# Optimization experiments

Hardware: AMD Instinct MI355X
Metric: run time of the kernel (lower is better)

## Reference

```python
import jax, jax.numpy as jnp
import numpy as np

B, C, H, W = 4, 3, 96, 96
HW = H * W
IGNORE = 0          # HD_IGNORE_CLASS_INDEX
BIG = 1e9           # stand-in for +inf in masked min


def setup_inputs() -> dict:
    key = jax.random.key(0)
    k1, k2 = jax.random.split(key)
    predictions = jax.random.normal(k1, (B, C, H, W), dtype=jnp.float32)
    labels_int = jax.random.randint(k2, (B, H, W), 0, C, dtype=jnp.int32)
    return {"predictions": predictions, "labels_int": labels_int}


def get_boundary(img):
    # img: [B, C, H, W] binary mask. Faithful to the numpy version (square images):
    # new = img + 4-neighbor sums (zero outside), boundary = img * (5 - new).
    pad = lambda x, spec: jnp.pad(x, ((0, 0), (0, 0)) + spec)
    new = (img
           + pad(img[:, :, 1:, :], ((0, 1), (0, 0)))
           + pad(img[:, :, :-1, :], ((1, 0), (0, 0)))
           + pad(img[:, :, :, 1:], ((0, 0), (0, 1)))
           + pad(img[:, :, :, :-1], ((0, 0), (1, 0))))
    return img * (5.0 - new)


def _pixel_dist_matrix():
    yy, xx = jnp.meshgrid(jnp.arange(H), jnp.arange(W), indexing="ij")
    coords = jnp.stack([yy.ravel(), xx.ravel()], axis=-1).astype(jnp.float32)  # [HW,2] (row,col) like argwhere
    sq = jnp.sum(coords * coords, axis=-1)
    D2 = sq[:, None] + sq[None, :] - 2.0 * (coords @ coords.T)
    return jnp.sqrt(jnp.maximum(D2, 0.0))  # [HW, HW]


def reference(predictions, labels_int):
    labels = jax.nn.one_hot(labels_int, C, axis=1, dtype=jnp.float32)        # [B,C,H,W]
    preds = jax.nn.one_hot(jnp.argmax(predictions, axis=1), C, axis=1,
                           dtype=jnp.float32)                                # [B,C,H,W]

    bd_a = (get_boundary(preds) > 0).astype(jnp.float32)
    bd_b = (get_boundary(labels) > 0).astype(jnp.float32)

    a = preds.reshape(B * C, HW)
    b = labels.reshape(B * C, HW)
    ba = bd_a.reshape(B * C, HW)
    bb = bd_b.reshape(B * C, HW)

    D = _pixel_dist_matrix()  # [HW, HW], shared across all (batch, class) pairs

    def pair(args):
        a_, b_, ba_, bb_ = args
        n_a = a_.sum()
        n_b = b_.sum()
        a_fwd = a_ * (1.0 - b_)   # pred-only pixels (false positive region)
        b_bwd = b_ * (1.0 - a_)   # label-only pixels
        # min distance from every pixel to boundary set, via masked min (no argwhere)
        mins_f = jnp.min(jnp.where(bb_[None, :] > 0, D, BIG), axis=1)  # to boundary(b)
        mins_b = jnp.min(jnp.where(ba_[None, :] > 0, D, BIG), axis=1)  # to boundary(a)
        # mean(min) * |A_fwd| / |a| == sum(min over A_fwd) / |a|
        hd_f = jnp.where((a_fwd.sum() > 0) & (bb_.sum() > 0),
                         jnp.sum(a_fwd * mins_f) / jnp.maximum(n_a, 1.0), 0.0)
        hd_b = jnp.where((b_bwd.sum() > 0) & (ba_.sum() > 0),
                         jnp.sum(b_bwd * mins_b) / jnp.maximum(n_b, 1.0), 0.0)
        hd = jnp.maximum(hd_f, hd_b)
        # empty prediction mask -> failure case (ignore_failed_hd = False => (h+w)/4)
        hd = jnp.where(n_a > 0, hd, (H + W) / 4.0)
        return hd, (n_a == 0).astype(jnp.float32)

    hd_pairs, failed_pairs = jax.lax.map(pair, (a, b, ba, bb))

    hd = hd_pairs.reshape(B, C).at[:, IGNORE].set(0.0)
    failed = failed_pairs.reshape(B, C).sum(axis=0).at[IGNORE].set(0.0)

    HD = jnp.zeros((B, C + 2), dtype=jnp.float32)
    HD = HD.at[:, :C].set(hd)
    HD = HD.at[:, C].set(jnp.mean(hd, axis=1))            # HD[:, -2] = mean over all C classes
    HD = HD.at[:, C + 1].set(jnp.mean(hd[:, :C - 1], axis=1))  # HD[:, -1] = mean over first C-1 (faithful to [:-3])

    Fc = jnp.zeros((C + 2,), dtype=jnp.float32)
    Fc = Fc.at[:C].set(failed)
    Fc = Fc.at[C].set(jnp.mean(failed))
    Fc = Fc.at[C + 1].set(jnp.mean(failed[1:C]))
    return HD, Fc
```

## Files before the change

kernel.cpp:

```cpp
#include <hip/hip_runtime.h>
#include <math.h>

namespace {
constexpr int Bn = 4, Cn = 3, Hn = 96, Wn = 96;
constexpr int HWn = Hn * Wn;
constexpr int NP  = Bn * Cn;
constexpr int NBLK1 = (Bn * HWn) / 256;
constexpr int SENT = 62500;

constexpr int FLAG_WORDS = Bn * HWn / 4;
constexpr int CNT_OFF  = FLAG_WORDS;
constexpr int NA_OFF   = CNT_OFF + NBLK1 * 8;
constexpr int NB_OFF   = NA_OFF + NP;
constexpr int SUM_OFF  = ((NB_OFF + NP + 15) / 16) * 16;
constexpr int SUM_WORDS = 2 * NP * 16;
constexpr int TICK_OFF = SUM_OFF + SUM_WORDS;
constexpr int ZERO_WORDS = SUM_WORDS + 16;
constexpr int MK_OFF   = TICK_OFF + 16;

__device__ __forceinline__ int SUMF_I(int pr) { return SUM_OFF + pr * 16; }
__device__ __forceinline__ int SUMB_I(int pr) { return SUM_OFF + (NP + pr) * 16; }
}

__global__ __launch_bounds__(256) void k_front(const float* __restrict__ preds,
                                               const int* __restrict__ labels,
                                               int* __restrict__ wi) {
    int blk = blockIdx.x, tid = threadIdx.x;
    int b = blk / 36;
    int p = (blk - b * 36) * 256 + tid;
    int y = p / Wn, x = p - y * Wn;
    const float* pb = preds + (size_t)b * Cn * HWn;
    const int*   lb = labels + b * HWn;

    auto amax = [&](int q) -> int {
        float v0 = pb[q], v1 = pb[HWn + q], v2 = pb[2 * HWn + q];
        int bi = 0; float bv = v0;
        if (v1 > bv) { bv = v1; bi = 1; }
        if (v2 > bv) { bv = v2; bi = 2; }
        return bi;
    };
    int pc = amax(p);
    int l  = lb[p];
    int ca = 0, cb = 0;
    if (y > 0)      { ca += (amax(p - Wn) == pc); cb += (lb[p - Wn] == l); }
    if (y < Hn - 1) { ca += (amax(p + Wn) == pc); cb += (lb[p + Wn] == l); }
    if (x > 0)      { ca += (amax(p - 1)  == pc); cb += (lb[p - 1]  == l); }
    if (x < Wn - 1) { ca += (amax(p + 1)  == pc); cb += (lb[p + 1]  == l); }
    ((unsigned char*)wi)[b * HWn + p] =
        (unsigned char)(pc | (l << 2) | ((ca < 4) << 4) | ((cb < 4) << 5));

    __shared__ int wcnt[4][6];
    int wv = tid >> 6, ln = tid & 63;
    int cnts[6];
#pragma unroll
    for (int c = 0; c < 3; ++c) {
        cnts[c]     = __popcll(__ballot(pc == c));
        cnts[3 + c] = __popcll(__ballot(l == c));
    }
    if (ln == 0) {
        for (int k = 0; k < 6; ++k) wcnt[wv][k] = cnts[k];
    }
    __syncthreads();
    if (tid < 6)
        wi[CNT_OFF + blk * 8 + tid] = wcnt[0][tid] + wcnt[1][tid] + wcnt[2][tid] + wcnt[3][tid];
    if (blk == 0) {
        if (tid < ZERO_WORDS) wi[SUM_OFF + tid] = 0;
        if (tid + 256 < ZERO_WORDS) wi[SUM_OFF + tid + 256] = 0;
    }
}

__global__ void k_masks(int* __restrict__ wi) {
    int t = blockIdx.x * blockDim.x + threadIdx.x;
    const unsigned char* flags = (const unsigned char*)wi;
    if (t < NP * 288) {
        int b = t / 864, rem = t - b * 864;
        int c = rem / 288, rem2 = rem - c * 288;
        int w = rem2 / 96, x = rem2 - w * 96;
        const unsigned char* fb = flags + b * HWn + x;
        unsigned am = 0, bm = 0;
#pragma unroll
        for (int k = 0; k < 32; ++k) {
            unsigned f = fb[(w * 32 + k) * Wn];
            am |= (unsigned)(((f >> 4) & 1) & (unsigned)((f & 3) == (unsigned)c)) << k;
            bm |= (unsigned)(((f >> 5) & 1) & (unsigned)(((f >> 2) & 3) == (unsigned)c)) << k;
        }
        int pr = b * Cn + c;
        wi[MK_OFF + pr * 576 + w * 96 + x]       = (int)am;
        wi[MK_OFF + pr * 576 + (w + 3) * 96 + x] = (int)bm;
    } else if (t < NP * 288 + 24) {
        int idx = t - NP * 288;
        int pr = idx % 12, which = idx / 12;
        int b = pr / Cn, c = pr - b * Cn;
        int s = 0;
        for (int k = 0; k < 36; ++k) s += wi[CNT_OFF + (b * 36 + k) * 8 + which * 3 + c];
        wi[(which ? NB_OFF : NA_OFF) + pr] = s;
    }
}

__global__ __launch_bounds__(384) void k_edt_sum(int* __restrict__ wi,
                                                 float* __restrict__ wf,
                                                 float* __restrict__ out) {
    int pr = blockIdx.y;
    int rb = blockIdx.x;
    int j  = threadIdx.x;
    int b = pr / Cn, c = pr - b * Cn;

    __shared__ unsigned int mlds[576];
    __shared__ unsigned int glds[384];
    __shared__ float sF6[6], sB6[6];
    __shared__ int lastflag;

    for (int k = j; k < 576; k += 384)
        mlds[k] = (unsigned int)wi[MK_OFF + pr * 576 + k];
    __syncthreads();

    int r = j / 96, xp = j - r * 96;
    int y = rb * 4 + r;

    unsigned long long alo = (unsigned long long)mlds[xp]
                           | ((unsigned long long)mlds[96 + xp] << 32);
    unsigned long long ahi = mlds[192 + xp];
    unsigned long long blo = (unsigned long long)mlds[288 + xp]
                           | ((unsigned long long)mlds[384 + xp] << 32);
    unsigned long long bhi = mlds[480 + xp];

    __uint128_t Ma = ((__uint128_t)ahi << 64) | alo;
    __uint128_t Mb = ((__uint128_t)bhi << 64) | blo;

    auto dist1d = [&](__uint128_t M) -> int {
        int du = 200, dd = 200;
        __uint128_t s = M >> y;
        if (s) {
            unsigned long long lo = (unsigned long long)s;
            du = lo ? __builtin_ctzll(lo) : 64 + __builtin_ctzll((unsigned long long)(s >> 64));
        }
        s = M << (127 - y);
        if (s) {
            unsigned long long h = (unsigned long long)(s >> 64);
            dd = h ? __builtin_clzll(h) : 64 + __builtin_clzll((unsigned long long)s);
        }
        int d = min(du, dd);
        return (d >= Hn) ? SENT : d * d;
    };
    glds[j] = (unsigned)dist1d(Mb) | ((unsigned)dist1d(Ma) << 16);
    __syncthreads();

    int p = y * Wn + xp;
    unsigned f = ((const unsigned char*)wi)[b * HWn + p];
    int a  = ((f & 3) == (unsigned)c);
    int bm = (((f >> 2) & 3) == (unsigned)c);
    int na = wi[NA_OFF + pr];
    int nb = wi[NB_OFF + pr];
    bool af = a && !bm && (nb > 0);
    bool bw = bm && !a && (na > 0);

    float s = 0.0f;
    if (af || bw) {
        int sh = af ? 0 : 16;
        int md2 = 0x7fffffff;
        const unsigned int* grow = &glds[r * 96];
#pragma unroll 8
        for (int q = 0; q < Wn; ++q) {
            int gs = (grow[q] >> sh) & 0xffff;
            int dx = xp - q;
            md2 = min(md2, gs + dx * dx);
        }
        s = sqrtf((float)md2);
    }
    float vF = af ? s : 0.0f;
    float vB = bw ? s : 0.0f;
#pragma unroll
    for (int off = 32; off >= 1; off >>= 1) {
        vF += __shfl_xor(vF, off, 64);
        vB += __shfl_xor(vB, off, 64);
    }
    int wv = j >> 6;
    if ((j & 63) == 0) { sF6[wv] = vF; sB6[wv] = vB; }
    __syncthreads();
    if (j == 0) {
        float t = sF6[0] + sF6[1] + sF6[2] + sF6[3] + sF6[4] + sF6[5];
        if (t != 0.0f) atomicAdd(&wf[SUMF_I(pr)], t);
    } else if (j == 64) {
        float t = sB6[0] + sB6[1] + sB6[2] + sB6[3] + sB6[4] + sB6[5];
        if (t != 0.0f) atomicAdd(&wf[SUMB_I(pr)], t);
    }

    __syncthreads();
    if (j == 0) {
        int old = atomicAdd(&wi[TICK_OFF], 1);
        lastflag = (old == NP * 24 - 1);
    }
    __syncthreads();
    if (!lastflag) return;

    __shared__ float hds[12];
    __shared__ float fld[12];
    if (j < 12) {
        int nA = wi[NA_OFF + j];
        int nB = wi[NB_OFF + j];
        float sFv = atomicAdd(&wf[SUMF_I(j)], 0.0f);
        float sBv = atomicAdd(&wf[SUMB_I(j)], 0.0f);
        float h, fl = 0.0f;
        if (nA == 0) { h = (Hn + Wn) / 4.0f; fl = 1.0f; }
        else {
            h = fmaxf(sFv / fmaxf((float)nA, 1.0f), sBv / fmaxf((float)nB, 1.0f));
        }
        if (j % Cn == 0) { h = 0.0f; fl = 0.0f; }
        hds[j] = h; fld[j] = fl;
    }
    __syncthreads();
    if (j == 0) {
        float failed[3] = {0.f, 0.f, 0.f};
        for (int q = 0; q < 12; ++q) failed[q % 3] += fld[q];
        for (int bb = 0; bb < Bn; ++bb) {
            float* row = out + bb * (Cn + 2);
            float ssum = 0.f;
            for (int cc = 0; cc < Cn; ++cc) { row[cc] = hds[bb * 3 + cc]; ssum += row[cc]; }
            row[Cn]     = ssum / (float)Cn;
            row[Cn + 1] = (hds[bb * 3] + hds[bb * 3 + 1]) / (float)(Cn - 1);
        }
        float* Fc = out + Bn * (Cn + 2);
        float fs = 0.f;
        for (int cc = 0; cc < Cn; ++cc) { Fc[cc] = failed[cc]; fs += failed[cc]; }
        Fc[Cn]     = fs / (float)Cn;
        Fc[Cn + 1] = (failed[1] + failed[2]) / (float)(Cn - 1);
    }
}

extern "C" void kernel_launch(void* const* d_in, const int* in_sizes, int n_in,
                              void* d_out, int out_size, void* d_ws, size_t ws_size,
                              hipStream_t stream) {
    const float* preds  = (const float*)d_in[0];
    const int*   labels = (const int*)d_in[1];
    float* out = (float*)d_out;
    int*   wi = (int*)d_ws;
    float* wf = (float*)d_ws;

    k_front<<<NBLK1, 256, 0, stream>>>(preds, labels, wi);
    k_masks<<<(NP * 288 + 24 + 255) / 256, 256, 0, stream>>>(wi);
    dim3 g3(Hn / 4, NP);
    k_edt_sum<<<g3, 384, 0, stream>>>(wi, wf, out);
}
```

Baseline: 69.55 us.

## Fuse mask packing into front kernel using LDS-tiled row bands

Merges k_masks into k_front. Each block now handles a 32-row band of one image: it stages argmax and label bytes (with halo rows) in LDS, computes boundary flags from shared memory, and builds the column bitmasks for that band directly from the LDS flags. The separate count-reduction pass is removed; the EDT kernel sums three per-band counts itself. This saves a kernel launch and the global round trip of the flags, at the cost of only 12 blocks for the front stage, which gives much less parallelism.

```diff
diff --git a/kernel.cpp b/kernel.cpp
--- a/kernel.cpp
+++ b/kernel.cpp
@@ -5,14 +5,13 @@
 constexpr int Bn = 4, Cn = 3, Hn = 96, Wn = 96;
 constexpr int HWn = Hn * Wn;
 constexpr int NP  = Bn * Cn;
-constexpr int NBLK1 = (Bn * HWn) / 256;
+constexpr int NBANDS = 3;
+constexpr int NBLK1 = Bn * NBANDS;
 constexpr int SENT = 62500;
 
 constexpr int FLAG_WORDS = Bn * HWn / 4;
 constexpr int CNT_OFF  = FLAG_WORDS;
-constexpr int NA_OFF   = CNT_OFF + NBLK1 * 8;
-constexpr int NB_OFF   = NA_OFF + NP;
-constexpr int SUM_OFF  = ((NB_OFF + NP + 15) / 16) * 16;
+constexpr int SUM_OFF  = ((CNT_OFF + NBLK1 * 8 + 15) / 16) * 16;
 constexpr int SUM_WORDS = 2 * NP * 16;
 constexpr int TICK_OFF = SUM_OFF + SUM_WORDS;
 constexpr int ZERO_WORDS = SUM_WORDS + 16;
@@ -22,78 +21,84 @@
 __device__ __forceinline__ int SUMB_I(int pr) { return SUM_OFF + (NP + pr) * 16; }
 }
 
-__global__ __launch_bounds__(256) void k_front(const float* __restrict__ preds,
+__global__ __launch_bounds__(384) void k_front(const float* __restrict__ preds,
                                                const int* __restrict__ labels,
                                                int* __restrict__ wi) {
-    int blk = blockIdx.x, tid = threadIdx.x;
-    int b = blk / 36;
-    int p = (blk - b * 36) * 256 + tid;
-    int y = p / Wn, x = p - y * Wn;
+    int blk = blockIdx.x, j = threadIdx.x;
+    int b = blk / NBANDS, w = blk - b * NBANDS;
+    int y0 = w * 32;
     const float* pb = preds + (size_t)b * Cn * HWn;
     const int*   lb = labels + b * HWn;
 
-    auto amax = [&](int q) -> int {
-        float v0 = pb[q], v1 = pb[HWn + q], v2 = pb[2 * HWn + q];
-        int bi = 0; float bv = v0;
-        if (v1 > bv) { bv = v1; bi = 1; }
-        if (v2 > bv) { bv = v2; bi = 2; }
-        return bi;
-    };
-    int pc = amax(p);
-    int l  = lb[p];
-    int ca = 0, cb = 0;
-    if (y > 0)      { ca += (amax(p - Wn) == pc); cb += (lb[p - Wn] == l); }
-    if (y < Hn - 1) { ca += (amax(p + Wn) == pc); cb += (lb[p + Wn] == l); }
-    if (x > 0)      { ca += (amax(p - 1)  == pc); cb += (lb[p - 1]  == l); }
-    if (x < Wn - 1) { ca += (amax(p + 1)  == pc); cb += (lb[p + 1]  == l); }
-    ((unsigned char*)wi)[b * HWn + p] =
-        (unsigned char)(pc | (l << 2) | ((ca < 4) << 4) | ((cb < 4) << 5));
-
-    __shared__ int wcnt[4][6];
-    int wv = tid >> 6, ln = tid & 63;
-    int cnts[6];
-#pragma unroll
-    for (int c = 0; c < 3; ++c) {
-        cnts[c]     = __popcll(__ballot(pc == c));
-        cnts[3 + c] = __popcll(__ballot(l == c));
-    }
-    if (ln == 0) {
-        for (int k = 0; k < 6; ++k) wcnt[wv][k] = cnts[k];
-    }
-    __syncthreads();
-    if (tid < 6)
-        wi[CNT_OFF + blk * 8 + tid] = wcnt[0][tid] + wcnt[1][tid] + wcnt[2][tid] + wcnt[3][tid];
+    __shared__ unsigned char apc[34 * 96];
+    __shared__ unsigned char albl[34 * 96];
+    __shared__ unsigned char aflg[32 * 96];
+    __shared__ int scnt[6];
+
+    if (j < 6) scnt[j] = 0;
+
+    for (int t = j; t < 34 * 96; t += 384) {
+        int r = t / 96, x = t - r * 96;
+        int y = y0 - 1 + r;
+        if ((unsigned)y < 96u) {
+            int p = y * Wn + x;
+            float v0 = pb[p], v1 = pb[HWn + p], v2 = pb[2 * HWn + p];
+            int bi = 0; float bv = v0;
+            if (v1 > bv) { bv = v1; bi = 1; }
+            if (v2 > bv) { bv = v2; bi = 2; }
+            apc[t]  = (unsigned char)bi;
+            albl[t] = (unsigned char)lb[p];
+        }
+    }
+    __syncthreads();
+
+    int cA[3] = {0, 0, 0}, cB[3] = {0, 0, 0};
+#pragma unroll
+    for (int k = 0; k < 8; ++k) {
+        int t = j + k * 384;
+        int r = t / 96, x = t - r * 96;
+        int y = y0 + r, ly = r + 1;
+        int pc = apc[ly * 96 + x], l = albl[ly * 96 + x];
+        int ca = 0, cb = 0;
+        if (y > 0)  { ca += (apc[(ly - 1) * 96 + x] == pc); cb += (albl[(ly - 1) * 96 + x] == l); }
+        if (y < 95) { ca += (apc[(ly + 1) * 96 + x] == pc); cb += (albl[(ly + 1) * 96 + x] == l); }
+        if (x > 0)  { ca += (apc[ly * 96 + x - 1] == pc);   cb += (albl[ly * 96 + x - 1] == l); }
+        if (x < 95) { ca += (apc[ly * 96 + x + 1] == pc);   cb += (albl[ly * 96 + x + 1] == l); }
+        unsigned char f = (unsigned char)(pc | (l << 2) | ((ca < 4) << 4) | ((cb < 4) << 5));
+        aflg[t] = f;
+        ((unsigned char*)wi)[b * HWn + y * Wn + x] = f;
+        cA[0] += (pc == 0); cA[1] += (pc == 1); cA[2] += (pc == 2);
+        cB[0] += (l == 0);  cB[1] += (l == 1);  cB[2] += (l == 2);
+    }
+    int vals[6] = {cA[0], cA[1], cA[2], cB[0], cB[1], cB[2]};
+#pragma unroll
+    for (int q = 0; q < 6; ++q) {
+        int v = vals[q];
+#pragma unroll
+        for (int off = 32; off >= 1; off >>= 1) v += __shfl_xor(v, off, 64);
+        if ((j & 63) == 0) atomicAdd(&scnt[q], v);
+    }
+    __syncthreads();
+
+    for (int k = j; k < 576; k += 384) {
+        int c = k / 192, rem = k - c * 192;
+        int which = rem / 96, x = rem - which * 96;
+        unsigned m = 0;
+#pragma unroll
+        for (int r = 0; r < 32; ++r) {
+            unsigned f = aflg[r * 96 + x];
+            unsigned bit = (which == 0)
+                ? (unsigned)(((f & 3) == (unsigned)c) & ((f >> 4) & 1))
+                : (unsigned)((((f >> 2) & 3) == (unsigned)c) & ((f >> 5) & 1));
+            m |= bit << r;
+        }
+        int pr = b * Cn + c;
+        wi[MK_OFF + pr * 576 + (which ? (w + 3) : w) * 96 + x] = (int)m;
+    }
+    if (j < 6) wi[CNT_OFF + blk * 8 + j] = scnt[j];
     if (blk == 0) {
-        if (tid < ZERO_WORDS) wi[SUM_OFF + tid] = 0;
-        if (tid + 256 < ZERO_WORDS) wi[SUM_OFF + tid + 256] = 0;
-    }
-}
-
-__global__ void k_masks(int* __restrict__ wi) {
-    int t = blockIdx.x * blockDim.x + threadIdx.x;
-    const unsigned char* flags = (const unsigned char*)wi;
-    if (t < NP * 288) {
-        int b = t / 864, rem = t - b * 864;
-        int c = rem / 288, rem2 = rem - c * 288;
-        int w = rem2 / 96, x = rem2 - w * 96;
-        const unsigned char* fb = flags + b * HWn + x;
-        unsigned am = 0, bm = 0;
-#pragma unroll
-        for (int k = 0; k < 32; ++k) {
-            unsigned f = fb[(w * 32 + k) * Wn];
-            am |= (unsigned)(((f >> 4) & 1) & (unsigned)((f & 3) == (unsigned)c)) << k;
-            bm |= (unsigned)(((f >> 5) & 1) & (unsigned)(((f >> 2) & 3) == (unsigned)c)) << k;
-        }
-        int pr = b * Cn + c;
-        wi[MK_OFF + pr * 576 + w * 96 + x]       = (int)am;
-        wi[MK_OFF + pr * 576 + (w + 3) * 96 + x] = (int)bm;
-    } else if (t < NP * 288 + 24) {
-        int idx = t - NP * 288;
-        int pr = idx % 12, which = idx / 12;
-        int b = pr / Cn, c = pr - b * Cn;
-        int s = 0;
-        for (int k = 0; k < 36; ++k) s += wi[CNT_OFF + (b * 36 + k) * 8 + which * 3 + c];
-        wi[(which ? NB_OFF : NA_OFF) + pr] = s;
+        if (j < ZERO_WORDS) wi[SUM_OFF + j] = 0;
+        if (j + 384 < ZERO_WORDS) wi[SUM_OFF + j + 384] = 0;
     }
 }
 
@@ -149,8 +154,12 @@
     unsigned f = ((const unsigned char*)wi)[b * HWn + p];
     int a  = ((f & 3) == (unsigned)c);
     int bm = (((f >> 2) & 3) == (unsigned)c);
-    int na = wi[NA_OFF + pr];
-    int nb = wi[NB_OFF + pr];
+    int na = wi[CNT_OFF + (b * NBANDS + 0) * 8 + c]
+           + wi[CNT_OFF + (b * NBANDS + 1) * 8 + c]
+           + wi[CNT_OFF + (b * NBANDS + 2) * 8 + c];
+    int nb = wi[CNT_OFF + (b * NBANDS + 0) * 8 + 3 + c]
+           + wi[CNT_OFF + (b * NBANDS + 1) * 8 + 3 + c]
+           + wi[CNT_OFF + (b * NBANDS + 2) * 8 + 3 + c];
     bool af = a && !bm && (nb > 0);
     bool bw = bm && !a && (na > 0);
 
@@ -196,8 +205,13 @@
     __shared__ float hds[12];
     __shared__ float fld[12];
     if (j < 12) {
-        int nA = wi[NA_OFF + j];
-        int nB = wi[NB_OFF + j];
+        int bb = j / Cn, cc = j - bb * Cn;
+        int nA = wi[CNT_OFF + (bb * NBANDS + 0) * 8 + cc]
+               + wi[CNT_OFF + (bb * NBANDS + 1) * 8 + cc]
+               + wi[CNT_OFF + (bb * NBANDS + 2) * 8 + cc];
+        int nB = wi[CNT_OFF + (bb * NBANDS + 0) * 8 + 3 + cc]
+               + wi[CNT_OFF + (bb * NBANDS + 1) * 8 + 3 + cc]
+               + wi[CNT_OFF + (bb * NBANDS + 2) * 8 + 3 + cc];
         float sFv = atomicAdd(&wf[SUMF_I(j)], 0.0f);
         float sBv = atomicAdd(&wf[SUMB_I(j)], 0.0f);
         float h, fl = 0.0f;
@@ -205,7 +219,7 @@
         else {
             h = fmaxf(sFv / fmaxf((float)nA, 1.0f), sBv / fmaxf((float)nB, 1.0f));
         }
-        if (j % Cn == 0) { h = 0.0f; fl = 0.0f; }
+        if (cc == 0) { h = 0.0f; fl = 0.0f; }
         hds[j] = h; fld[j] = fl;
     }
     __syncthreads();
@@ -236,8 +250,7 @@
     int*   wi = (int*)d_ws;
     float* wf = (float*)d_ws;
 
-    k_front<<<NBLK1, 256, 0, stream>>>(preds, labels, wi);
-    k_masks<<<(NP * 288 + 24 + 255) / 256, 256, 0, stream>>>(wi);
-    dim3 g3(Hn / 4, NP);
-    k_edt_sum<<<g3, 384, 0, stream>>>(wi, wf, out);
-}
+    k_front<<<NBLK1, 384, 0, stream>>>(preds, labels, wi);
+    dim3 g2(Hn / 4, NP);
+    k_edt_sum<<<g2, 384, 0, stream>>>(wi, wf, out);
+}
```

Result: slower. 74.80 us (+7.6%).
